# Optimization experiments

Measured on AMD Instinct MI355X. Metric: run time of the kernel, lower is better.

The kernel has to match this reference:

```python
import jax, jax.numpy as jnp
import numpy as np
from jax import lax

D_MODEL = 1024
D_STATE = 16
D_CONV = 4
EXPAND = 2
D_INNER = EXPAND * D_MODEL            # 2048
DT_RANK = (D_MODEL + 15) // 16        # 64
B, L = 2, 2048
EPS = 1e-5


def setup_inputs() -> dict:
    key = jax.random.key(0)
    ks = jax.random.split(key, 12)
    s = 0.02
    x = jax.random.normal(ks[0], (B, L, D_MODEL), dtype=jnp.float32)
    norm_w = jnp.ones((D_MODEL,), dtype=jnp.float32)
    in_proj_w = jax.random.normal(ks[1], (2 * D_INNER, D_MODEL), dtype=jnp.float32) * s
    conv_w = jax.random.normal(ks[2], (D_INNER, D_CONV), dtype=jnp.float32) * 0.1
    conv_b = jax.random.normal(ks[3], (D_INNER,), dtype=jnp.float32) * 0.01
    x_proj_w = jax.random.normal(ks[4], (DT_RANK + 2 * D_STATE, D_INNER), dtype=jnp.float32) * s
    dt_proj_w = jax.random.normal(ks[5], (D_INNER, DT_RANK), dtype=jnp.float32) * 0.1
    dt_proj_b = jax.random.normal(ks[6], (D_INNER,), dtype=jnp.float32) * 0.5 - 4.0  # small softplus(delta)
    # S4D-real init: A = -(1..d_state) per channel
    A_log = jnp.log(jnp.broadcast_to(jnp.arange(1, D_STATE + 1, dtype=jnp.float32), (D_INNER, D_STATE)))
    Dp = jnp.ones((D_INNER,), dtype=jnp.float32)
    out_proj_w = jax.random.normal(ks[7], (D_MODEL, D_INNER), dtype=jnp.float32) * s
    return {"x": x, "norm_w": norm_w, "in_proj_w": in_proj_w, "conv_w": conv_w,
            "conv_b": conv_b, "x_proj_w": x_proj_w, "dt_proj_w": dt_proj_w,
            "dt_proj_b": dt_proj_b, "A_log": A_log, "Dp": Dp, "out_proj_w": out_proj_w}


def _selective_scan(deltaA, deltaBu, Cm):
    # deltaA, deltaBu: [B,L,Di,N]; Cm: [B,L,N] -> y: [B,L,Di]
    def step(h, inp):
        dA, dBu, c = inp
        h = dA * h + dBu                       # [B,Di,N]
        y = jnp.einsum('bdn,bn->bd', h, c)     # [B,Di]
        return h, y
    h0 = jnp.zeros(deltaA.shape[0:1] + deltaA.shape[2:], deltaA.dtype)
    _, ys = lax.scan(step, h0, (deltaA.transpose(1, 0, 2, 3),
                                deltaBu.transpose(1, 0, 2, 3),
                                Cm.transpose(1, 0, 2)))
    return ys.transpose(1, 0, 2)               # [B,L,Di]


def reference(x, norm_w, in_proj_w, conv_w, conv_b, x_proj_w,
              dt_proj_w, dt_proj_b, A_log, Dp, out_proj_w):
    d_inner, d_conv = conv_w.shape
    d_state = A_log.shape[1]
    dt_rank = dt_proj_w.shape[1]

    # RMSNorm
    rms = jnp.sqrt(jnp.mean(x * x, axis=-1, keepdims=True) + EPS)
    xn = norm_w * (x / rms)

    # input projection -> x, z streams
    xz = jnp.einsum('bld,ed->ble', xn, in_proj_w)      # [B,L,2*Di]
    xi, z = jnp.split(xz, 2, axis=-1)

    # depthwise causal conv1d + SiLU
    xc = lax.conv_general_dilated(
        xi.transpose(0, 2, 1), conv_w[:, None, :], (1,), [(d_conv - 1, 0)],
        dimension_numbers=('NCL', 'OIL', 'NCL'), feature_group_count=d_inner)
    xc = jax.nn.silu(xc.transpose(0, 2, 1) + conv_b)   # [B,L,Di]

    # input-dependent SSM params
    dbl = jnp.einsum('bld,ed->ble', xc, x_proj_w)      # [B,L,dt_rank+2N]
    dt, Bm, Cm = jnp.split(dbl, [dt_rank, dt_rank + d_state], axis=-1)
    delta = jax.nn.softplus(jnp.einsum('blr,dr->bld', dt, dt_proj_w) + dt_proj_b)

    A = -jnp.exp(A_log)                                # [Di,N]
    deltaA = jnp.exp(delta[..., None] * A)             # [B,L,Di,N]
    deltaBu = delta[..., None] * Bm[:, :, None, :] * xc[..., None]

    y = _selective_scan(deltaA, deltaBu, Cm)           # [B,L,Di]
    y = y + xc * Dp
    y = y * jax.nn.silu(z)

    out = jnp.einsum('bld,ed->ble', y, out_proj_w)     # [B,L,d_model]
    return x + out
```

## Files before the change

### kernel.cpp

```cpp
#include <hip/hip_runtime.h>
#include <hip/hip_bf16.h>
#include <math.h>

#define D_MODEL 1024
#define D_STATE 16
#define D_CONV 4
#define D_INNER 2048
#define DT_RANK 64
#define BATCH 2
#define SEQ 2048
#define NTOK (BATCH*SEQ)
#define EPS 1e-5f
#define CCH 32
#define TCH (SEQ/CCH)
#define XKS 8
#define XKC (D_INNER/XKS)

typedef __attribute__((ext_vector_type(8))) short short8;
typedef __attribute__((ext_vector_type(4))) float f32x4;
typedef __attribute__((ext_vector_type(4))) unsigned short us4;

__device__ inline unsigned short f2bf(float f) {
  union { __hip_bfloat16 h; unsigned short u; } c;
  c.h = __float2bfloat16(f);
  return c.u;
}
__device__ inline float bf2f(unsigned short u) {
  union { unsigned int i; float f; } c;
  c.i = ((unsigned int)u) << 16;
  return c.f;
}

#define GLL(gp, lp) __builtin_amdgcn_global_load_lds( \
    (const __attribute__((address_space(1))) void*)(gp), \
    (__attribute__((address_space(3))) void*)(lp), 16, 0, 0)

__global__ __launch_bounds__(256) void f2bf4_kernel(
    const float* __restrict__ i0, unsigned short* __restrict__ o0, int b0,
    const float* __restrict__ i1, unsigned short* __restrict__ o1, int b1,
    const float* __restrict__ i2, unsigned short* __restrict__ o2, int b2,
    const float* __restrict__ i3, unsigned short* __restrict__ o3)
{
  int blk = blockIdx.x;
  const float* in; unsigned short* out; int base;
  if (blk < b0)           { in = i0; out = o0; base = blk; }
  else if (blk < b0+b1)   { in = i1; out = o1; base = blk - b0; }
  else if (blk < b0+b1+b2){ in = i2; out = o2; base = blk - b0 - b1; }
  else                    { in = i3; out = o3; base = blk - b0 - b1 - b2; }
  int i = (base*256 + threadIdx.x)*4;
  float4 v = *(const float4*)(in + i);
  us4 o;
  o[0] = f2bf(v.x); o[1] = f2bf(v.y); o[2] = f2bf(v.z); o[3] = f2bf(v.w);
  *(us4*)(out + i) = o;
}

__global__ __launch_bounds__(256) void rmsnorm_kernel(const float* __restrict__ x,
                                                      const float* __restrict__ w,
                                                      unsigned short* __restrict__ xn) {
  int tok = blockIdx.x;
  const float* xr = x + (size_t)tok * D_MODEL;
  unsigned short* xo = xn + (size_t)tok * D_MODEL;
  int t = threadIdx.x;
  float4 v = ((const float4*)xr)[t];
  float ss = v.x*v.x + v.y*v.y + v.z*v.z + v.w*v.w;
  #pragma unroll
  for (int off = 32; off > 0; off >>= 1) ss += __shfl_down(ss, off, 64);
  __shared__ float wsum[4];
  __shared__ float rinv_s;
  int lane = t & 63, wv = t >> 6;
  if (lane == 0) wsum[wv] = ss;
  __syncthreads();
  if (t == 0) {
    float tot = wsum[0] + wsum[1] + wsum[2] + wsum[3];
    rinv_s = 1.0f / sqrtf(tot / (float)D_MODEL + EPS);
  }
  __syncthreads();
  float rinv = rinv_s;
  float4 g = ((const float4*)w)[t];
  us4 o;
  o[0] = f2bf(v.x * rinv * g.x);
  o[1] = f2bf(v.y * rinv * g.y);
  o[2] = f2bf(v.z * rinv * g.z);
  o[3] = f2bf(v.w * rinv * g.w);
  *(us4*)(xo + t*4) = o;
}

template<int NT>
__global__ __launch_bounds__(512) void gemm256_bf16_kernel(
    const unsigned short* __restrict__ A,
    const unsigned short* __restrict__ W,
    unsigned short* __restrict__ C, int ldc)
{
  const int K = NT*64;
  __shared__ __align__(16) unsigned short As[2][16384];
  __shared__ __align__(16) unsigned short Bs[2][16384];
  int tid = threadIdx.x;
  int lane = tid & 63;
  int w = tid >> 6;
  int wm = w >> 2, wn = w & 3;
  int bm = blockIdx.x * 256;
  int bn = blockIdx.y * 256;
  int r15 = lane & 15, g8 = (lane >> 4) * 8;
  int rbh0 = (w & 3) + (w >> 2) * 8;
  int rbh1 = rbh0 + 4;

  auto stageA = [&](int slot, int tile, int ks, int rb) {
    const unsigned short* src = A + (size_t)(bm + rb*16 + r15) * K + tile*64 + ks*32 + g8;
    GLL(src, &As[slot][rb*1024 + ks*512]);
  };
  auto stageB = [&](int slot, int tile, int ks, int cb) {
    const unsigned short* src = W + (size_t)(bn + cb*16 + r15) * K + tile*64 + ks*32 + g8;
    GLL(src, &Bs[slot][cb*1024 + ks*512]);
  };

  stageA(0,0,0,rbh0); stageB(0,0,0,w); stageB(0,0,0,8+w);
  stageA(0,0,0,rbh1);
  stageA(0,0,1,rbh0); stageB(0,0,1,w); stageB(0,0,1,8+w);
  stageA(0,0,1,rbh1);
  stageA(1,1,0,rbh0); stageB(1,1,0,w); stageB(1,1,0,8+w);
  stageA(1,1,0,rbh1);
  stageA(1,1,1,rbh0); stageB(1,1,1,w); stageB(1,1,1,8+w);
  asm volatile("s_waitcnt vmcnt(7)" ::: "memory");
  __builtin_amdgcn_s_barrier();
  __builtin_amdgcn_sched_barrier(0);

  f32x4 acc[8][4] = {};
  short8 bfr[4];

#define PHASE_END()                                                      \
  if (drain) { asm volatile("s_waitcnt vmcnt(0)" ::: "memory"); }        \
  else       { asm volatile("s_waitcnt vmcnt(12)" ::: "memory"); }       \
  __builtin_amdgcn_s_barrier();                                          \
  __builtin_amdgcn_sched_barrier(0);

#define MFMA16(IH)                                                       \
  __builtin_amdgcn_s_setprio(1);                                         \
  _Pragma("unroll")                                                      \
  for (int ii = 0; ii < 4; ++ii) {                                       \
    _Pragma("unroll")                                                    \
    for (int j = 0; j < 4; ++j)                                          \
      acc[(IH)*4+ii][j] = __builtin_amdgcn_mfma_f32_16x16x32_bf16(       \
          af[ii], bfr[j], acc[(IH)*4+ii][j], 0, 0, 0);                   \
  }                                                                      \
  __builtin_amdgcn_s_setprio(0);

#define LOAD_A(KS, IH)                                                   \
  short8 af[4];                                                          \
  _Pragma("unroll")                                                      \
  for (int ii = 0; ii < 4; ++ii)                                         \
    af[ii] = *(const short8*)&As[s][(wm*8 + (IH)*4 + ii)*1024 + (KS)*512 + lane*8];

#define LOAD_B(KS)                                                       \
  _Pragma("unroll")                                                      \
  for (int j = 0; j < 4; ++j)                                            \
    bfr[j] = *(const short8*)&Bs[s][(wn*4 + j)*1024 + (KS)*512 + lane*8];

  for (int t = 0; t < NT; ++t) {
    int s = t & 1;
    const bool drain = (t >= NT-2);
    {
      LOAD_A(0,0)
      LOAD_B(0)
      if (t+1 < NT) { stageA(s^1, t+1, 1, rbh1); }
      MFMA16(0)
      PHASE_END()
    }
    {
      LOAD_A(0,1)
      if (t+2 < NT) { stageA(s, t+2, 0, rbh0); stageB(s, t+2, 0, w); stageB(s, t+2, 0, 8+w); }
      MFMA16(1)
      PHASE_END()
    }
    {
      LOAD_A(1,0)
      LOAD_B(1)
      if (t+2 < NT) { stageA(s, t+2, 0, rbh1); }
      MFMA16(0)
      PHASE_END()
    }
    {
      LOAD_A(1,1)
      if (t+2 < NT) { stageA(s, t+2, 1, rbh0); stageB(s, t+2, 1, w); stageB(s, t+2, 1, 8+w); }
      MFMA16(1)
      PHASE_END()
    }
  }
#undef PHASE_END
#undef MFMA16
#undef LOAD_A
#undef LOAD_B

  #pragma unroll
  for (int ig = 0; ig < 8; ++ig) {
    #pragma unroll
    for (int j = 0; j < 4; ++j) {
      #pragma unroll
      for (int r = 0; r < 4; ++r) {
        int row = bm + wm*128 + ig*16 + (lane >> 4)*4 + r;
        int col = bn + wn*64 + j*16 + r15;
        C[(size_t)row * ldc + col] = f2bf(acc[ig][j][r]);
      }
    }
  }
}

template<int EPI, int OBF>
__global__ __launch_bounds__(256) void gemm_bf16_kernel(
    const unsigned short* __restrict__ A,
    const unsigned short* __restrict__ W,
    void* __restrict__ Cv, int ldc, int K,
    const float* __restrict__ bias,
    const float* __restrict__ resid)
{
  __shared__ __align__(16) unsigned short Abuf[8*64*8];
  __shared__ __align__(16) unsigned short Bbuf[8*64*8];
  int tid = threadIdx.x;
  int lane = tid & 63;
  int w = tid >> 6;
  int bm = blockIdx.x * 128;
  int bn = blockIdx.y * 128;
  int wrow = (w >> 1) * 64;
  int wcol = (w & 1) * 64;

  int r15 = lane & 15, g = lane >> 4;
  const unsigned short* Ag0 = A + (size_t)(bm + 2*w*16 + r15) * K + g*8;
  const unsigned short* Ag1 = Ag0 + (size_t)16 * K;
  const unsigned short* Wg0 = W + (size_t)(bn + 2*w*16 + r15) * K + g*8;
  const unsigned short* Wg1 = Wg0 + (size_t)16 * K;
  unsigned short* Al0 = &Abuf[(2*w  )*512];
  unsigned short* Al1 = &Abuf[(2*w+1)*512];
  unsigned short* Bl0 = &Bbuf[(2*w  )*512];
  unsigned short* Bl1 = &Bbuf[(2*w+1)*512];

  f32x4 acc[4][4] = {};

  for (int k0 = 0; k0 < K; k0 += 32) {
    __syncthreads();
    GLL(Ag0 + k0, Al0);
    GLL(Ag1 + k0, Al1);
    GLL(Wg0 + k0, Bl0);
    GLL(Wg1 + k0, Bl1);
    __syncthreads();

    short8 af[4], bfr[4];
    #pragma unroll
    for (int i = 0; i < 4; ++i)
      af[i] = *(const short8*)&Abuf[((wrow >> 4) + i)*512 + lane*8];
    #pragma unroll
    for (int j = 0; j < 4; ++j)
      bfr[j] = *(const short8*)&Bbuf[((wcol >> 4) + j)*512 + lane*8];
    #pragma unroll
    for (int i = 0; i < 4; ++i)
      #pragma unroll
      for (int j = 0; j < 4; ++j)
        acc[i][j] = __builtin_amdgcn_mfma_f32_16x16x32_bf16(af[i], bfr[j], acc[i][j], 0, 0, 0);
  }

  #pragma unroll
  for (int i = 0; i < 4; ++i) {
    #pragma unroll
    for (int j = 0; j < 4; ++j) {
      #pragma unroll
      for (int r = 0; r < 4; ++r) {
        int row = bm + wrow + i*16 + (lane >> 4)*4 + r;
        int col = bn + wcol + j*16 + (lane & 15);
        float v = acc[i][j][r];
        if (EPI == 1) {
          float s = v + bias[col];
          v = fmaxf(s, 0.f) + log1pf(__expf(-fabsf(s)));
        } else if (EPI == 2) {
          v += resid[(size_t)row * ldc + col];
        }
        if (OBF) ((unsigned short*)Cv)[(size_t)row * ldc + col] = f2bf(v);
        else     ((float*)Cv)[(size_t)row * ldc + col] = v;
      }
    }
  }
}

__global__ __launch_bounds__(256) void xproj_bf16_kernel(
    const unsigned short* __restrict__ A,
    const unsigned short* __restrict__ W,
    float* __restrict__ Ppart)
{
  __shared__ __align__(16) unsigned short Abuf[8*512];
  __shared__ __align__(16) unsigned short Bbuf[6*512];
  int tid = threadIdx.x;
  int lane = tid & 63;
  int w = tid >> 6;
  int bm = blockIdx.x * 128;
  int kc = blockIdx.y;
  const int K = D_INNER;
  int r15 = lane & 15, g = lane >> 4;

  const unsigned short* Ag0 = A + (size_t)(bm + 2*w*16 + r15) * K + g*8 + kc*XKC;
  const unsigned short* Ag1 = Ag0 + (size_t)16 * K;
  const unsigned short* Wg0 = W + (size_t)(w*16 + r15) * K + g*8 + kc*XKC;
  const unsigned short* Wg1 = W + (size_t)((4+w)*16 + r15) * K + g*8 + kc*XKC;
  unsigned short* Al0 = &Abuf[(2*w  )*512];
  unsigned short* Al1 = &Abuf[(2*w+1)*512];
  unsigned short* Bl0 = &Bbuf[w*512];
  unsigned short* Bl1 = &Bbuf[(4+w)*512];

  f32x4 acc[2][6] = {};

  for (int k0 = 0; k0 < XKC; k0 += 32) {
    __syncthreads();
    GLL(Ag0 + k0, Al0);
    GLL(Ag1 + k0, Al1);
    GLL(Wg0 + k0, Bl0);
    if (w < 2) GLL(Wg1 + k0, Bl1);
    __syncthreads();

    short8 af[2], bfr[6];
    #pragma unroll
    for (int i = 0; i < 2; ++i)
      af[i] = *(const short8*)&Abuf[(2*w + i)*512 + lane*8];
    #pragma unroll
    for (int j = 0; j < 6; ++j)
      bfr[j] = *(const short8*)&Bbuf[j*512 + lane*8];
    #pragma unroll
    for (int i = 0; i < 2; ++i)
      #pragma unroll
      for (int j = 0; j < 6; ++j)
        acc[i][j] = __builtin_amdgcn_mfma_f32_16x16x32_bf16(af[i], bfr[j], acc[i][j], 0, 0, 0);
  }

  float* out = Ppart + (size_t)kc * NTOK * 96;
  #pragma unroll
  for (int i = 0; i < 2; ++i) {
    #pragma unroll
    for (int j = 0; j < 6; ++j) {
      #pragma unroll
      for (int r = 0; r < 4; ++r) {
        int row = bm + w*32 + i*16 + (lane >> 4)*4 + r;
        int col = j*16 + (lane & 15);
        out[(size_t)row * 96 + col] = acc[i][j][r];
      }
    }
  }
}

__global__ __launch_bounds__(256) void xproj_reduce_kernel(
    const float* __restrict__ Ppart, float* __restrict__ dbl,
    unsigned short* __restrict__ dtbf)
{
  int idx = blockIdx.x * 256 + threadIdx.x;
  float s = 0.f;
  #pragma unroll
  for (int k = 0; k < XKS; ++k) s += Ppart[(size_t)k * NTOK * 96 + idx];
  dbl[idx] = s;
  int row = idx / 96, col = idx - row * 96;
  if (col < DT_RANK) dtbf[(size_t)row * DT_RANK + col] = f2bf(s);
}

__global__ __launch_bounds__(256) void conv_silu_kernel(
    const unsigned short* __restrict__ xz, const float* __restrict__ cw,
    const float* __restrict__ cb, unsigned short* __restrict__ xcbf)
{
  int idx = blockIdx.x * 256 + threadIdx.x;
  int dq = idx & (D_INNER/4 - 1);
  int tok = idx >> 9;
  int l = tok & (SEQ - 1);
  int d = dq * 4;
  const unsigned short* xi = xz + (size_t)tok * (2*D_INNER) + d;
  us4 v3 = *(const us4*)xi;
  us4 v2 = l >= 1 ? *(const us4*)(xi - 1*(2*D_INNER)) : (us4)0;
  us4 v1 = l >= 2 ? *(const us4*)(xi - 2*(2*D_INNER)) : (us4)0;
  us4 v0 = l >= 3 ? *(const us4*)(xi - 3*(2*D_INNER)) : (us4)0;
  float4 cbv = *(const float4*)(cb + d);
  float cbx[4] = {cbv.x, cbv.y, cbv.z, cbv.w};
  us4 o;
  #pragma unroll
  for (int j = 0; j < 4; ++j) {
    float4 wv = *(const float4*)(cw + (d + j) * 4);
    float s = cbx[j];
    s = fmaf(bf2f(v0[j]), wv.x, s);
    s = fmaf(bf2f(v1[j]), wv.y, s);
    s = fmaf(bf2f(v2[j]), wv.z, s);
    s = fmaf(bf2f(v3[j]), wv.w, s);
    float v = s / (1.f + __expf(-s));
    o[j] = f2bf(v);
  }
  *(us4*)(xcbf + (size_t)tok * D_INNER + d) = o;
}

__global__ __launch_bounds__(256) void scan_pass1(
    const unsigned short* __restrict__ delta, const float* __restrict__ dbl,
    const unsigned short* __restrict__ xc, const float* __restrict__ A_log,
    float* __restrict__ P, float* __restrict__ He)
{
  int blk = blockIdx.x;
  int d = (blk & 7) * 256 + threadIdx.x;
  int c = (blk >> 3) & (CCH - 1);
  int b = blk >> 8;
  float Adn[16];
  #pragma unroll
  for (int n = 0; n < 16; ++n) Adn[n] = -__expf(A_log[d*16 + n]);
  float h[16] = {};
  float sdl = 0.f;
  int tok0 = b * SEQ + c * TCH;
  for (int t = 0; t < TCH; ++t) {
    size_t tok = (size_t)(tok0 + t);
    float dl = bf2f(delta[tok * D_INNER + d]);
    float xcv = bf2f(xc[tok * D_INNER + d]);
    float u = dl * xcv;
    const float4* bp = (const float4*)(dbl + tok*96 + 64);
    float4 b0 = bp[0], b1 = bp[1], b2 = bp[2], b3 = bp[3];
    float bv[16] = {b0.x,b0.y,b0.z,b0.w, b1.x,b1.y,b1.z,b1.w,
                    b2.x,b2.y,b2.z,b2.w, b3.x,b3.y,b3.z,b3.w};
    sdl += dl;
    #pragma unroll
    for (int n = 0; n < 16; ++n)
      h[n] = fmaf(__expf(dl * Adn[n]), h[n], u * bv[n]);
  }
  size_t base = ((size_t)(b*CCH + c) * 16) * D_INNER + d;
  #pragma unroll
  for (int n = 0; n < 16; ++n) {
    P [base + (size_t)n * D_INNER] = __expf(Adn[n] * sdl);
    He[base + (size_t)n * D_INNER] = h[n];
  }
}

__global__ __launch_bounds__(256) void scan_pass2(
    const float* __restrict__ P, const float* __restrict__ He,
    float* __restrict__ Hin)
{
  int blk = blockIdx.x;
  int d = (blk & 7) * 256 + threadIdx.x;
  int n = (blk >> 3) & 15;
  int b = blk >> 7;
  float h = 0.f;
  #pragma unroll 4
  for (int c = 0; c < CCH; ++c) {
    size_t idx = ((size_t)(b*CCH + c) * 16 + n) * D_INNER + d;
    Hin[idx] = h;
    h = fmaf(P[idx], h, He[idx]);
  }
}

__global__ __launch_bounds__(256) void scan_pass3(
    const unsigned short* __restrict__ delta, const float* __restrict__ dbl,
    const unsigned short* __restrict__ xc, const unsigned short* __restrict__ xz,
    const float* __restrict__ A_log, const float* __restrict__ Dp,
    const float* __restrict__ Hin, unsigned short* __restrict__ y)
{
  int blk = blockIdx.x;
  int d = (blk & 7) * 256 + threadIdx.x;
  int c = (blk >> 3) & (CCH - 1);
  int b = blk >> 8;
  float Adn[16];
  #pragma unroll
  for (int n = 0; n < 16; ++n) Adn[n] = -__expf(A_log[d*16 + n]);
  float Dpd = Dp[d];
  float h[16];
  size_t base = ((size_t)(b*CCH + c) * 16) * D_INNER + d;
  #pragma unroll
  for (int n = 0; n < 16; ++n) h[n] = Hin[base + (size_t)n * D_INNER];
  int tok0 = b * SEQ + c * TCH;
  for (int t = 0; t < TCH; ++t) {
    size_t tok = (size_t)(tok0 + t);
    float dl = bf2f(delta[tok * D_INNER + d]);
    float xcv = bf2f(xc[tok * D_INNER + d]);
    float u = dl * xcv;
    const float4* bp = (const float4*)(dbl + tok*96 + 64);
    float4 b0 = bp[0], b1 = bp[1], b2 = bp[2], b3 = bp[3];
    float4 c0 = bp[4], c1 = bp[5], c2 = bp[6], c3 = bp[7];
    float bv[16] = {b0.x,b0.y,b0.z,b0.w, b1.x,b1.y,b1.z,b1.w,
                    b2.x,b2.y,b2.z,b2.w, b3.x,b3.y,b3.z,b3.w};
    float cv[16] = {c0.x,c0.y,c0.z,c0.w, c1.x,c1.y,c1.z,c1.w,
                    c2.x,c2.y,c2.z,c2.w, c3.x,c3.y,c3.z,c3.w};
    float z = bf2f(xz[tok * (2*D_INNER) + D_INNER + d]);
    float acc = xcv * Dpd;
    #pragma unroll
    for (int n = 0; n < 16; ++n) {
      h[n] = fmaf(__expf(dl * Adn[n]), h[n], u * bv[n]);
      acc = fmaf(h[n], cv[n], acc);
    }
    float sz = z / (1.f + __expf(-z));
    y[tok * D_INNER + d] = f2bf(acc * sz);
  }
}

extern "C" void kernel_launch(void* const* d_in, const int* in_sizes, int n_in,
                              void* d_out, int out_size, void* d_ws, size_t ws_size,
                              hipStream_t stream) {
  const float* x         = (const float*)d_in[0];
  const float* norm_w    = (const float*)d_in[1];
  const float* in_proj_w = (const float*)d_in[2];
  const float* conv_w    = (const float*)d_in[3];
  const float* conv_b    = (const float*)d_in[4];
  const float* x_proj_w  = (const float*)d_in[5];
  const float* dt_proj_w = (const float*)d_in[6];
  const float* dt_proj_b = (const float*)d_in[7];
  const float* A_log     = (const float*)d_in[8];
  const float* Dp        = (const float*)d_in[9];
  const float* out_proj_w= (const float*)d_in[10];
  float* out = (float*)d_out;

  char* ws = (char*)d_ws;
  unsigned short* xz_bf   = (unsigned short*)(ws);
  unsigned short* xc_bf   = (unsigned short*)(ws + ( 32ull<<20));
  float*          dbl     = (float*)(ws + ( 48ull<<20));
  unsigned short* delta_bf= (unsigned short*)(ws + ( 50ull<<20));
  unsigned short* xn_bf   = (unsigned short*)(ws + ( 66ull<<20));
  unsigned short* w_in_bf = (unsigned short*)(ws + ( 74ull<<20));
  unsigned short* w_out_bf= (unsigned short*)(ws + ( 82ull<<20));
  unsigned short* w_xp_bf = (unsigned short*)(ws + ( 86ull<<20));
  unsigned short* w_dt_bf = (unsigned short*)(ws + ( 87ull<<20));
  unsigned short* dtbf    = (unsigned short*)(ws + ( 88ull<<20));
  float*          Ppart   = (float*)(ws + ( 89ull<<20));
  float*          Pst     = (float*)(ws + (102ull<<20));
  float*          Hest    = (float*)(ws + (110ull<<20));
  float*          Hin     = (float*)(ws + (118ull<<20));
  unsigned short* yb_bf   = (unsigned short*)(ws + (126ull<<20));

  rmsnorm_kernel<<<NTOK, 256, 0, stream>>>(x, norm_w, xn_bf);

  f2bf4_kernel<<<4096+2048+192+128, 256, 0, stream>>>(
      in_proj_w, w_in_bf, 4096,
      out_proj_w, w_out_bf, 2048,
      x_proj_w, w_xp_bf, 192,
      dt_proj_w, w_dt_bf);

  {
    dim3 g(NTOK/256, (2*D_INNER)/256);
    gemm256_bf16_kernel<D_MODEL/64><<<g, 512, 0, stream>>>(xn_bf, w_in_bf, xz_bf, 2*D_INNER);
  }

  conv_silu_kernel<<<(NTOK*D_INNER/4)/256, 256, 0, stream>>>(xz_bf, conv_w, conv_b, xc_bf);

  {
    dim3 g(NTOK/128, XKS);
    xproj_bf16_kernel<<<g, 256, 0, stream>>>(xc_bf, w_xp_bf, Ppart);
    xproj_reduce_kernel<<<(NTOK*96)/256, 256, 0, stream>>>(Ppart, dbl, dtbf);
  }

  {
    dim3 g(NTOK/128, D_INNER/128);
    gemm_bf16_kernel<1,1><<<g, 256, 0, stream>>>(dtbf, w_dt_bf, delta_bf, D_INNER, DT_RANK,
                                                 dt_proj_b, nullptr);
  }

  scan_pass1<<<BATCH*CCH*8, 256, 0, stream>>>(delta_bf, dbl, xc_bf, A_log, Pst, Hest);
  scan_pass2<<<BATCH*16*8, 256, 0, stream>>>(Pst, Hest, Hin);
  scan_pass3<<<BATCH*CCH*8, 256, 0, stream>>>(delta_bf, dbl, xc_bf, xz_bf, A_log, Dp, Hin, yb_bf);

  {
    dim3 g(NTOK/128, D_MODEL/128);
    gemm_bf16_kernel<2,0><<<g, 256, 0, stream>>>(yb_bf, w_out_bf, out, D_MODEL, D_INNER,
                                                 nullptr, x);
  }
}
```

Measured before the change: 350.6 us.

## Double-buffer LDS in GEMM and x_proj kernels; add dedicated dt_proj kernel

Converts the bf16 GEMM and x_proj kernels to double-buffered shared memory, so the next K tile's global-to-LDS load is issued while MFMAs run on the current tile. This replaces two barriers per iteration with one. Separately, the dt_proj GEMM (K=64) moves off the MFMA tile kernel onto a scalar FMA kernel, where each block handles 8 tokens against 1024 channels with the softplus fused in. The costs are doubled LDS usage, which may lower occupancy, and heavy per-thread weight reloads in the new dt kernel.

Result: slower. 411.1 us (+17.3%).

```diff
diff --git a/kernel.cpp b/kernel.cpp
--- a/kernel.cpp
+++ b/kernel.cpp
@@ -209,11 +209,10 @@
     const unsigned short* __restrict__ A,
     const unsigned short* __restrict__ W,
     void* __restrict__ Cv, int ldc, int K,
-    const float* __restrict__ bias,
     const float* __restrict__ resid)
 {
-  __shared__ __align__(16) unsigned short Abuf[8*64*8];
-  __shared__ __align__(16) unsigned short Bbuf[8*64*8];
+  __shared__ __align__(16) unsigned short Abuf[2][4096];
+  __shared__ __align__(16) unsigned short Bbuf[2][4096];
   int tid = threadIdx.x;
   int lane = tid & 63;
   int w = tid >> 6;
@@ -227,33 +226,39 @@
   const unsigned short* Ag1 = Ag0 + (size_t)16 * K;
   const unsigned short* Wg0 = W + (size_t)(bn + 2*w*16 + r15) * K + g*8;
   const unsigned short* Wg1 = Wg0 + (size_t)16 * K;
-  unsigned short* Al0 = &Abuf[(2*w  )*512];
-  unsigned short* Al1 = &Abuf[(2*w+1)*512];
-  unsigned short* Bl0 = &Bbuf[(2*w  )*512];
-  unsigned short* Bl1 = &Bbuf[(2*w+1)*512];
+
+  auto STAGE = [&](int slot, int t) {
+    int k0 = t * 32;
+    GLL(Ag0 + k0, &Abuf[slot][(2*w  )*512]);
+    GLL(Ag1 + k0, &Abuf[slot][(2*w+1)*512]);
+    GLL(Wg0 + k0, &Bbuf[slot][(2*w  )*512]);
+    GLL(Wg1 + k0, &Bbuf[slot][(2*w+1)*512]);
+  };
 
   f32x4 acc[4][4] = {};
-
-  for (int k0 = 0; k0 < K; k0 += 32) {
-    __syncthreads();
-    GLL(Ag0 + k0, Al0);
-    GLL(Ag1 + k0, Al1);
-    GLL(Wg0 + k0, Bl0);
-    GLL(Wg1 + k0, Bl1);
-    __syncthreads();
+  const int nt = K / 32;
+
+  STAGE(0, 0);
+  __syncthreads();
+
+  for (int t = 0; t < nt; ++t) {
+    int s = t & 1;
+    if (t + 1 < nt) STAGE(s ^ 1, t + 1);
 
     short8 af[4], bfr[4];
     #pragma unroll
     for (int i = 0; i < 4; ++i)
-      af[i] = *(const short8*)&Abuf[((wrow >> 4) + i)*512 + lane*8];
+      af[i] = *(const short8*)&Abuf[s][((wrow >> 4) + i)*512 + lane*8];
     #pragma unroll
     for (int j = 0; j < 4; ++j)
-      bfr[j] = *(const short8*)&Bbuf[((wcol >> 4) + j)*512 + lane*8];
+      bfr[j] = *(const short8*)&Bbuf[s][((wcol >> 4) + j)*512 + lane*8];
     #pragma unroll
     for (int i = 0; i < 4; ++i)
       #pragma unroll
       for (int j = 0; j < 4; ++j)
         acc[i][j] = __builtin_amdgcn_mfma_f32_16x16x32_bf16(af[i], bfr[j], acc[i][j], 0, 0, 0);
+
+    __syncthreads();
   }
 
   #pragma unroll
@@ -265,12 +270,7 @@
         int row = bm + wrow + i*16 + (lane >> 4)*4 + r;
         int col = bn + wcol + j*16 + (lane & 15);
         float v = acc[i][j][r];
-        if (EPI == 1) {
-          float s = v + bias[col];
-          v = fmaxf(s, 0.f) + log1pf(__expf(-fabsf(s)));
-        } else if (EPI == 2) {
-          v += resid[(size_t)row * ldc + col];
-        }
+        if (EPI == 2) v += resid[(size_t)row * ldc + col];
         if (OBF) ((unsigned short*)Cv)[(size_t)row * ldc + col] = f2bf(v);
         else     ((float*)Cv)[(size_t)row * ldc + col] = v;
       }
@@ -283,8 +283,8 @@
     const unsigned short* __restrict__ W,
     float* __restrict__ Ppart)
 {
-  __shared__ __align__(16) unsigned short Abuf[8*512];
-  __shared__ __align__(16) unsigned short Bbuf[6*512];
+  __shared__ __align__(16) unsigned short Abuf[2][4096];
+  __shared__ __align__(16) unsigned short Bbuf[2][3072];
   int tid = threadIdx.x;
   int lane = tid & 63;
   int w = tid >> 6;
@@ -297,33 +297,39 @@
   const unsigned short* Ag1 = Ag0 + (size_t)16 * K;
   const unsigned short* Wg0 = W + (size_t)(w*16 + r15) * K + g*8 + kc*XKC;
   const unsigned short* Wg1 = W + (size_t)((4+w)*16 + r15) * K + g*8 + kc*XKC;
-  unsigned short* Al0 = &Abuf[(2*w  )*512];
-  unsigned short* Al1 = &Abuf[(2*w+1)*512];
-  unsigned short* Bl0 = &Bbuf[w*512];
-  unsigned short* Bl1 = &Bbuf[(4+w)*512];
+
+  auto STAGE = [&](int slot, int t) {
+    int k0 = t * 32;
+    GLL(Ag0 + k0, &Abuf[slot][(2*w  )*512]);
+    GLL(Ag1 + k0, &Abuf[slot][(2*w+1)*512]);
+    GLL(Wg0 + k0, &Bbuf[slot][w*512]);
+    if (w < 2) GLL(Wg1 + k0, &Bbuf[slot][(4+w)*512]);
+  };
 
   f32x4 acc[2][6] = {};
-
-  for (int k0 = 0; k0 < XKC; k0 += 32) {
-    __syncthreads();
-    GLL(Ag0 + k0, Al0);
-    GLL(Ag1 + k0, Al1);
-    GLL(Wg0 + k0, Bl0);
-    if (w < 2) GLL(Wg1 + k0, Bl1);
-    __syncthreads();
+  const int nt = XKC / 32;
+
+  STAGE(0, 0);
+  __syncthreads();
+
+  for (int t = 0; t < nt; ++t) {
+    int s = t & 1;
+    if (t + 1 < nt) STAGE(s ^ 1, t + 1);
 
     short8 af[2], bfr[6];
     #pragma unroll
     for (int i = 0; i < 2; ++i)
-      af[i] = *(const short8*)&Abuf[(2*w + i)*512 + lane*8];
+      af[i] = *(const short8*)&Abuf[s][(2*w + i)*512 + lane*8];
     #pragma unroll
     for (int j = 0; j < 6; ++j)
-      bfr[j] = *(const short8*)&Bbuf[j*512 + lane*8];
+      bfr[j] = *(const short8*)&Bbuf[s][j*512 + lane*8];
     #pragma unroll
     for (int i = 0; i < 2; ++i)
       #pragma unroll
       for (int j = 0; j < 6; ++j)
         acc[i][j] = __builtin_amdgcn_mfma_f32_16x16x32_bf16(af[i], bfr[j], acc[i][j], 0, 0, 0);
+
+    __syncthreads();
   }
 
   float* out = Ppart + (size_t)kc * NTOK * 96;
@@ -352,6 +358,55 @@
   dbl[idx] = s;
   int row = idx / 96, col = idx - row * 96;
   if (col < DT_RANK) dtbf[(size_t)row * DT_RANK + col] = f2bf(s);
+}
+
+__global__ __launch_bounds__(256) void dtproj_kernel(
+    const unsigned short* __restrict__ dtbf,
+    const unsigned short* __restrict__ Wdt,
+    const float* __restrict__ bias,
+    unsigned short* __restrict__ delta)
+{
+  __shared__ float dt_s[8*64];
+  int tg = blockIdx.x;
+  int cg = blockIdx.y;
+  int tid = threadIdx.x;
+  if (tid < 128) {
+    us4 v = *(const us4*)(dtbf + (size_t)tg*8*64 + tid*4);
+    #pragma unroll
+    for (int i = 0; i < 4; ++i) dt_s[tid*4 + i] = bf2f(v[i]);
+  }
+  __syncthreads();
+  int lane = tid & 63, w = tid >> 6;
+  #pragma unroll
+  for (int q = 0; q < 4; ++q) {
+    int d = cg*1024 + w*256 + q*64 + lane;
+    short8 wv[8];
+    #pragma unroll
+    for (int rg = 0; rg < 8; ++rg)
+      wv[rg] = *(const short8*)(Wdt + (size_t)d*64 + rg*8);
+    float bd = bias[d];
+    float s[8];
+    #pragma unroll
+    for (int tok = 0; tok < 8; ++tok) s[tok] = bd;
+    #pragma unroll
+    for (int rg = 0; rg < 8; ++rg) {
+      float wf[8];
+      #pragma unroll
+      for (int j = 0; j < 8; ++j) wf[j] = bf2f((unsigned short)wv[rg][j]);
+      #pragma unroll
+      for (int tok = 0; tok < 8; ++tok) {
+        const float* dp = &dt_s[tok*64 + rg*8];
+        #pragma unroll
+        for (int j = 0; j < 8; ++j) s[tok] = fmaf(dp[j], wf[j], s[tok]);
+      }
+    }
+    #pragma unroll
+    for (int tok = 0; tok < 8; ++tok) {
+      float v = s[tok];
+      float sp = fmaxf(v, 0.f) + log1pf(__expf(-fabsf(v)));
+      delta[(size_t)(tg*8 + tok) * D_INNER + d] = f2bf(sp);
+    }
+  }
 }
 
 __global__ __launch_bounds__(256) void conv_silu_kernel(
@@ -537,9 +592,8 @@
   }
 
   {
-    dim3 g(NTOK/128, D_INNER/128);
-    gemm_bf16_kernel<1,1><<<g, 256, 0, stream>>>(dtbf, w_dt_bf, delta_bf, D_INNER, DT_RANK,
-                                                 dt_proj_b, nullptr);
+    dim3 g(NTOK/8, 2);
+    dtproj_kernel<<<g, 256, 0, stream>>>(dtbf, w_dt_bf, dt_proj_b, delta_bf);
   }
 
   scan_pass1<<<BATCH*CCH*8, 256, 0, stream>>>(delta_bf, dbl, xc_bf, A_log, Pst, Hest);
@@ -548,7 +602,6 @@
 
   {
     dim3 g(NTOK/128, D_MODEL/128);
-    gemm_bf16_kernel<2,0><<<g, 256, 0, stream>>>(yb_bf, w_out_bf, out, D_MODEL, D_INNER,
-                                                 nullptr, x);
-  }
-}
+    gemm_bf16_kernel<2,0><<<g, 256, 0, stream>>>(yb_bf, w_out_bf, out, D_MODEL, D_INNER, x);
+  }
+}
```
